# Kernel optimization log

Hardware: AMD Instinct MI355X
Metric: run time of the kernel (lower is better)

The kernel has to match this reference:

```python
import jax, jax.numpy as jnp
import numpy as np

ORDER = 7
MEMORY_DEPTH = 4
LAG_DEPTH = 2
B, S = 8, 65536


def _delay(sig, d):
    # prepend d zeros, drop last d samples (tf.concat-based delay in source)
    if d == 0:
        return sig
    return jnp.concatenate([jnp.zeros((d,), dtype=sig.dtype), sig[:-d]], axis=0)


def _setup_basis_matrix(x):
    # x: [N] complex64 -> [N, n_coeffs] complex64 (GMP basis)
    abs_x = jnp.abs(x)
    step = 2  # odd orders only (use_even=False)
    cols = []
    # main memory-polynomial terms: x * |x|^(k-1), delayed 0..M-1
    for order in range(1, ORDER + 1, step):
        branch = x * (abs_x ** (order - 1)).astype(x.dtype)
        for d in range(MEMORY_DEPTH):
            cols.append(_delay(branch, d))
    # lagging cross-terms: x * |x|^(k-1) shifted later by `lag`
    for order in range(3, ORDER + 1, step):
        abs_base = abs_x ** (order - 1)
        for lag in range(1, LAG_DEPTH + 1):
            lagged = jnp.concatenate(
                [jnp.zeros((lag,), dtype=abs_base.dtype), abs_base[:-lag]], axis=0)
            branch = x * lagged.astype(x.dtype)
            for d in range(MEMORY_DEPTH):
                cols.append(_delay(branch, d))
    # leading cross-terms: x * |x|^(k-1) shifted earlier by `lead`
    for order in range(3, ORDER + 1, step):
        abs_base = abs_x ** (order - 1)
        for lead in range(1, LAG_DEPTH + 1):
            led = jnp.concatenate(
                [abs_base[lead:], jnp.zeros((lead,), dtype=abs_base.dtype)], axis=0)
            branch = x * led.astype(x.dtype)
            for d in range(MEMORY_DEPTH):
                cols.append(_delay(branch, d))
    return jnp.stack(cols, axis=1)  # [N, 64]


def setup_inputs() -> dict:
    key = jax.random.key(0)
    k1, k2, k3, k4 = jax.random.split(key, 4)
    x_real = jax.random.normal(k1, (B, S), dtype=jnp.float32) * 0.3
    x_imag = jax.random.normal(k2, (B, S), dtype=jnp.float32) * 0.3
    # layer init is delta coeffs (coeffs[0]=1); use small random perturbation
    # around it so gradients are non-trivial
    coeffs_real = jax.random.normal(k3, (64, 1), dtype=jnp.float32) * 0.01
    coeffs_real = coeffs_real.at[0, 0].add(1.0)
    coeffs_imag = jax.random.normal(k4, (64, 1), dtype=jnp.float32) * 0.01
    return {"x_real": x_real, "x_imag": x_imag,
            "coeffs_real": coeffs_real, "coeffs_imag": coeffs_imag}


def reference(x_real, x_imag, coeffs_real, coeffs_imag):
    # predistort() on 2D input: flatten, build basis over the whole flat
    # signal, matmul with complex coeffs, reshape back to [B, S]
    x = (x_real + 1j * x_imag).reshape(-1).astype(jnp.complex64)  # [N]
    coeffs = (coeffs_real + 1j * coeffs_imag).astype(jnp.complex64)  # [64, 1]
    X = _setup_basis_matrix(x)  # [N, 64]
    y = (X @ coeffs).reshape(-1)  # [N]
    return y.reshape(x_real.shape)  # [B, S] complex64
```

## Files before the change

kernel.cpp:

```cpp
#include <hip/hip_runtime.h>


constexpr int BLOCK  = 256;
constexpr int HALO_L = 5;
constexpr int HALO_R = 2;
constexpr int TILE   = BLOCK + HALO_L + HALO_R;

__global__ __launch_bounds__(BLOCK) void dpd_gmp_kernel(
    const float* __restrict__ xr, const float* __restrict__ xi,
    const float* __restrict__ cr, const float* __restrict__ ci,
    float* __restrict__ out, int N, int out_size)
{
    __shared__ float sxr[TILE];
    __shared__ float sxi[TILE];

    const int tid  = threadIdx.x;
    const int base = blockIdx.x * BLOCK;

    for (int k = tid; k < TILE; k += BLOCK) {
        int m = base - HALO_L + k;
        bool ok = (m >= 0) && (m < N);
        sxr[k] = ok ? xr[m] : 0.0f;
        sxi[k] = ok ? xi[m] : 0.0f;
    }
    __syncthreads();

    const int n = base + tid;

    float wr[8], wi[8], p2[8], p4[8], p6[8];
#pragma unroll
    for (int w = 0; w < 8; ++w) {
        wr[w] = sxr[tid + w];
        wi[w] = sxi[tid + w];
        float s = wr[w] * wr[w] + wi[w] * wi[w];
        p2[w] = s;
        p4[w] = s * s;
        p6[w] = p4[w] * s;
    }

    float yr = 0.0f, yi = 0.0f;
#pragma unroll
    for (int d = 0; d < 4; ++d) {
        const int i = HALO_L - d;

        float Cr = cr[0 + d];
        float Ci = ci[0 + d];
        Cr = fmaf(cr[ 4 + d], p2[i],     Cr);  Ci = fmaf(ci[ 4 + d], p2[i],     Ci);
        Cr = fmaf(cr[ 8 + d], p4[i],     Cr);  Ci = fmaf(ci[ 8 + d], p4[i],     Ci);
        Cr = fmaf(cr[12 + d], p6[i],     Cr);  Ci = fmaf(ci[12 + d], p6[i],     Ci);
        Cr = fmaf(cr[16 + d], p2[i - 1], Cr);  Ci = fmaf(ci[16 + d], p2[i - 1], Ci);
        Cr = fmaf(cr[20 + d], p2[i - 2], Cr);  Ci = fmaf(ci[20 + d], p2[i - 2], Ci);
        Cr = fmaf(cr[24 + d], p4[i - 1], Cr);  Ci = fmaf(ci[24 + d], p4[i - 1], Ci);
        Cr = fmaf(cr[28 + d], p4[i - 2], Cr);  Ci = fmaf(ci[28 + d], p4[i - 2], Ci);
        Cr = fmaf(cr[32 + d], p6[i - 1], Cr);  Ci = fmaf(ci[32 + d], p6[i - 1], Ci);
        Cr = fmaf(cr[36 + d], p6[i - 2], Cr);  Ci = fmaf(ci[36 + d], p6[i - 2], Ci);
        Cr = fmaf(cr[40 + d], p2[i + 1], Cr);  Ci = fmaf(ci[40 + d], p2[i + 1], Ci);
        Cr = fmaf(cr[44 + d], p2[i + 2], Cr);  Ci = fmaf(ci[44 + d], p2[i + 2], Ci);
        Cr = fmaf(cr[48 + d], p4[i + 1], Cr);  Ci = fmaf(ci[48 + d], p4[i + 1], Ci);
        Cr = fmaf(cr[52 + d], p4[i + 2], Cr);  Ci = fmaf(ci[52 + d], p4[i + 2], Ci);
        Cr = fmaf(cr[56 + d], p6[i + 1], Cr);  Ci = fmaf(ci[56 + d], p6[i + 1], Ci);
        Cr = fmaf(cr[60 + d], p6[i + 2], Cr);  Ci = fmaf(ci[60 + d], p6[i + 2], Ci);

        yr = fmaf(wr[i],  Cr, yr);
        yr = fmaf(-wi[i], Ci, yr);
        yi = fmaf(wr[i],  Ci, yi);
        yi = fmaf(wi[i],  Cr, yi);
    }

    if (n < N) {
        if (n < out_size)     out[n]     = yr;
        if (N + n < out_size) out[N + n] = yi;
    }
}

extern "C" void kernel_launch(void* const* d_in, const int* in_sizes, int n_in,
                              void* d_out, int out_size, void* d_ws, size_t ws_size,
                              hipStream_t stream) {
    const float* xr = (const float*)d_in[0];
    const float* xi = (const float*)d_in[1];
    const float* cr = (const float*)d_in[2];
    const float* ci = (const float*)d_in[3];
    float* out = (float*)d_out;

    const int N = in_sizes[0];
    const int grid = (N + BLOCK - 1) / BLOCK;
    dpd_gmp_kernel<<<grid, BLOCK, 0, stream>>>(xr, xi, cr, ci, out, N, out_size);
}
```

Before: 63.93 us.

## Process four samples per thread with vectorized float4 loads and stores

Each thread now computes four consecutive outputs, sharing an 11-sample register window of powers so |x|^k terms are reused across outputs instead of recomputed per thread. Interior blocks load the shared-memory tile with float4 loads, and outputs are written as float4 stores. The grid shrinks by four, which cuts the halo overhead per sample and the count of global transactions, at the cost of more registers per thread and fewer blocks in flight.

```diff
diff --git a/kernel.cpp b/kernel.cpp
--- a/kernel.cpp
+++ b/kernel.cpp
@@ -2,74 +2,105 @@
 
 
 constexpr int BLOCK  = 256;
-constexpr int HALO_L = 5;
-constexpr int HALO_R = 2;
-constexpr int TILE   = BLOCK + HALO_L + HALO_R;
+constexpr int VPT    = 4;
+constexpr int SAMP   = BLOCK * VPT;
+constexpr int HALO_L = 8;
+constexpr int HALO_R = 4;
+constexpr int TILE   = SAMP + HALO_L + HALO_R;
+constexpr int TILE4  = TILE / 4;
 
 __global__ __launch_bounds__(BLOCK) void dpd_gmp_kernel(
     const float* __restrict__ xr, const float* __restrict__ xi,
     const float* __restrict__ cr, const float* __restrict__ ci,
     float* __restrict__ out, int N, int out_size)
 {
-    __shared__ float sxr[TILE];
-    __shared__ float sxi[TILE];
+    __shared__ __align__(16) float sxr[TILE];
+    __shared__ __align__(16) float sxi[TILE];
 
     const int tid  = threadIdx.x;
-    const int base = blockIdx.x * BLOCK;
+    const int base = blockIdx.x * SAMP;
 
-    for (int k = tid; k < TILE; k += BLOCK) {
-        int m = base - HALO_L + k;
-        bool ok = (m >= 0) && (m < N);
-        sxr[k] = ok ? xr[m] : 0.0f;
-        sxi[k] = ok ? xi[m] : 0.0f;
+    const bool interior = (base >= HALO_L) && (base + SAMP + HALO_R <= N);
+    if (interior) {
+        const float4* xr4 = reinterpret_cast<const float4*>(xr + base - HALO_L);
+        const float4* xi4 = reinterpret_cast<const float4*>(xi + base - HALO_L);
+        float4* sr4 = reinterpret_cast<float4*>(sxr);
+        float4* si4 = reinterpret_cast<float4*>(sxi);
+        for (int f = tid; f < TILE4; f += BLOCK) {
+            sr4[f] = xr4[f];
+            si4[f] = xi4[f];
+        }
+    } else {
+        for (int k = tid; k < TILE; k += BLOCK) {
+            int m = base - HALO_L + k;
+            bool ok = (m >= 0) && (m < N);
+            sxr[k] = ok ? xr[m] : 0.0f;
+            sxi[k] = ok ? xi[m] : 0.0f;
+        }
     }
     __syncthreads();
 
-    const int n = base + tid;
+    const int n0 = base + tid * VPT;
+    const int l0 = tid * VPT + HALO_L - 5;
 
-    float wr[8], wi[8], p2[8], p4[8], p6[8];
+    float wr[11], wi[11], p2[11], p4[11], p6[11];
 #pragma unroll
-    for (int w = 0; w < 8; ++w) {
-        wr[w] = sxr[tid + w];
-        wi[w] = sxi[tid + w];
-        float s = wr[w] * wr[w] + wi[w] * wi[w];
-        p2[w] = s;
-        p4[w] = s * s;
-        p6[w] = p4[w] * s;
+    for (int j = 0; j < 11; ++j) {
+        wr[j] = sxr[l0 + j];
+        wi[j] = sxi[l0 + j];
+        float s = wr[j] * wr[j] + wi[j] * wi[j];
+        p2[j] = s;
+        p4[j] = s * s;
+        p6[j] = p4[j] * s;
     }
 
-    float yr = 0.0f, yi = 0.0f;
+    float yr[VPT], yi[VPT];
 #pragma unroll
-    for (int d = 0; d < 4; ++d) {
-        const int i = HALO_L - d;
+    for (int o = 0; o < VPT; ++o) { yr[o] = 0.0f; yi[o] = 0.0f; }
 
-        float Cr = cr[0 + d];
-        float Ci = ci[0 + d];
-        Cr = fmaf(cr[ 4 + d], p2[i],     Cr);  Ci = fmaf(ci[ 4 + d], p2[i],     Ci);
-        Cr = fmaf(cr[ 8 + d], p4[i],     Cr);  Ci = fmaf(ci[ 8 + d], p4[i],     Ci);
-        Cr = fmaf(cr[12 + d], p6[i],     Cr);  Ci = fmaf(ci[12 + d], p6[i],     Ci);
-        Cr = fmaf(cr[16 + d], p2[i - 1], Cr);  Ci = fmaf(ci[16 + d], p2[i - 1], Ci);
-        Cr = fmaf(cr[20 + d], p2[i - 2], Cr);  Ci = fmaf(ci[20 + d], p2[i - 2], Ci);
-        Cr = fmaf(cr[24 + d], p4[i - 1], Cr);  Ci = fmaf(ci[24 + d], p4[i - 1], Ci);
-        Cr = fmaf(cr[28 + d], p4[i - 2], Cr);  Ci = fmaf(ci[28 + d], p4[i - 2], Ci);
-        Cr = fmaf(cr[32 + d], p6[i - 1], Cr);  Ci = fmaf(ci[32 + d], p6[i - 1], Ci);
-        Cr = fmaf(cr[36 + d], p6[i - 2], Cr);  Ci = fmaf(ci[36 + d], p6[i - 2], Ci);
-        Cr = fmaf(cr[40 + d], p2[i + 1], Cr);  Ci = fmaf(ci[40 + d], p2[i + 1], Ci);
-        Cr = fmaf(cr[44 + d], p2[i + 2], Cr);  Ci = fmaf(ci[44 + d], p2[i + 2], Ci);
-        Cr = fmaf(cr[48 + d], p4[i + 1], Cr);  Ci = fmaf(ci[48 + d], p4[i + 1], Ci);
-        Cr = fmaf(cr[52 + d], p4[i + 2], Cr);  Ci = fmaf(ci[52 + d], p4[i + 2], Ci);
-        Cr = fmaf(cr[56 + d], p6[i + 1], Cr);  Ci = fmaf(ci[56 + d], p6[i + 1], Ci);
-        Cr = fmaf(cr[60 + d], p6[i + 2], Cr);  Ci = fmaf(ci[60 + d], p6[i + 2], Ci);
+#pragma unroll
+    for (int o = 0; o < VPT; ++o) {
+#pragma unroll
+        for (int d = 0; d < 4; ++d) {
+            const int i = 5 + o - d;
 
-        yr = fmaf(wr[i],  Cr, yr);
-        yr = fmaf(-wi[i], Ci, yr);
-        yi = fmaf(wr[i],  Ci, yi);
-        yi = fmaf(wi[i],  Cr, yi);
+            float Cr = cr[0 + d];
+            float Ci = ci[0 + d];
+            Cr = fmaf(cr[ 4 + d], p2[i],     Cr);  Ci = fmaf(ci[ 4 + d], p2[i],     Ci);
+            Cr = fmaf(cr[ 8 + d], p4[i],     Cr);  Ci = fmaf(ci[ 8 + d], p4[i],     Ci);
+            Cr = fmaf(cr[12 + d], p6[i],     Cr);  Ci = fmaf(ci[12 + d], p6[i],     Ci);
+            Cr = fmaf(cr[16 + d], p2[i - 1], Cr);  Ci = fmaf(ci[16 + d], p2[i - 1], Ci);
+            Cr = fmaf(cr[20 + d], p2[i - 2], Cr);  Ci = fmaf(ci[20 + d], p2[i - 2], Ci);
+            Cr = fmaf(cr[24 + d], p4[i - 1], Cr);  Ci = fmaf(ci[24 + d], p4[i - 1], Ci);
+            Cr = fmaf(cr[28 + d], p4[i - 2], Cr);  Ci = fmaf(ci[28 + d], p4[i - 2], Ci);
+            Cr = fmaf(cr[32 + d], p6[i - 1], Cr);  Ci = fmaf(ci[32 + d], p6[i - 1], Ci);
+            Cr = fmaf(cr[36 + d], p6[i - 2], Cr);  Ci = fmaf(ci[36 + d], p6[i - 2], Ci);
+            Cr = fmaf(cr[40 + d], p2[i + 1], Cr);  Ci = fmaf(ci[40 + d], p2[i + 1], Ci);
+            Cr = fmaf(cr[44 + d], p2[i + 2], Cr);  Ci = fmaf(ci[44 + d], p2[i + 2], Ci);
+            Cr = fmaf(cr[48 + d], p4[i + 1], Cr);  Ci = fmaf(ci[48 + d], p4[i + 1], Ci);
+            Cr = fmaf(cr[52 + d], p4[i + 2], Cr);  Ci = fmaf(ci[52 + d], p4[i + 2], Ci);
+            Cr = fmaf(cr[56 + d], p6[i + 1], Cr);  Ci = fmaf(ci[56 + d], p6[i + 1], Ci);
+            Cr = fmaf(cr[60 + d], p6[i + 2], Cr);  Ci = fmaf(ci[60 + d], p6[i + 2], Ci);
+
+            yr[o] = fmaf(wr[i],  Cr, yr[o]);
+            yr[o] = fmaf(-wi[i], Ci, yr[o]);
+            yi[o] = fmaf(wr[i],  Ci, yi[o]);
+            yi[o] = fmaf(wi[i],  Cr, yi[o]);
+        }
     }
 
-    if (n < N) {
-        if (n < out_size)     out[n]     = yr;
-        if (N + n < out_size) out[N + n] = yi;
+    if (n0 + VPT <= N && N + n0 + VPT <= out_size) {
+        *reinterpret_cast<float4*>(out + n0)     = make_float4(yr[0], yr[1], yr[2], yr[3]);
+        *reinterpret_cast<float4*>(out + N + n0) = make_float4(yi[0], yi[1], yi[2], yi[3]);
+    } else {
+#pragma unroll
+        for (int o = 0; o < VPT; ++o) {
+            int n = n0 + o;
+            if (n < N) {
+                if (n < out_size)     out[n]     = yr[o];
+                if (N + n < out_size) out[N + n] = yi[o];
+            }
+        }
     }
 }
 
@@ -83,6 +114,6 @@
     float* out = (float*)d_out;
 
     const int N = in_sizes[0];
-    const int grid = (N + BLOCK - 1) / BLOCK;
+    const int grid = (N + SAMP - 1) / SAMP;
     dpd_gmp_kernel<<<grid, BLOCK, 0, stream>>>(xr, xi, cr, ci, out, N, out_size);
 }
```

Result: slower. 67.96 us (+6.3%).
